# Performance work log

Measured on AMD Instinct MI355X. Metric: run time of the kernel, lower is better.

## Reference

```python
import jax, jax.numpy as jnp
import numpy as np

INFERENCE_TH = 0.3


def setup_inputs() -> dict:
    key = jax.random.key(0)
    k1, k2 = jax.random.split(key)
    N, C, H, W, K = 16, 30, 128, 128, 1000
    # Shift logits down so sigmoid scores are sparse above the threshold (realistic detector output).
    sCls = jax.random.normal(k1, (N, C, H, W), dtype=jnp.float32) - 2.0
    sReg = jax.random.normal(k2, (N, C * 16, H, W), dtype=jnp.float32) * 0.1
    # Anchors on a stride-8 grid, 64x64 boxes, laid out row-major to match the [N,H,W,A,C] flatten order.
    ys, xs = jnp.meshgrid(jnp.arange(H, dtype=jnp.float32) * 8.0 + 4.0,
                          jnp.arange(W, dtype=jnp.float32) * 8.0 + 4.0, indexing='ij')
    cx = xs.reshape(-1); cy = ys.reshape(-1); s = 32.0
    anchors = jnp.stack([cx - s, cy - s, cx + s, cy + s], axis=-1)  # [HW, 4]
    return {"sCls": sCls, "sReg": sReg, "anchors": anchors, "top_k": K}


def reference(sCls, sReg, anchors, top_k):
    N, C, H, W = sCls.shape
    HW = H * W
    # permute_and_flatten: [N, A*C, H, W] -> [N, H*W*A, C]  (A == 1)
    cls = jax.nn.sigmoid(jnp.transpose(sCls, (0, 2, 3, 1)).reshape(N, HW, C))        # [N, HW, C]
    reg = jnp.transpose(sReg, (0, 2, 3, 1)).reshape(N, HW, C, 16)                    # [N, HW, C, 16]
    # candidate_inds nonzero ordering is (loc, class) row-major over [HW, C];
    # flat index = loc*C + class, so topk over the flat axis reproduces it.
    flat = cls.reshape(N, HW * C)
    masked = jnp.where(flat > INFERENCE_TH, flat, -1.0)
    topv, topi = jax.lax.top_k(masked, top_k)        # [N, K]
    valid = topv > INFERENCE_TH                      # emulates per_pre_ransac_top_n truncation
    loc = topi // C                                  # spatial location (per_loc)
    cls_id = topi % C                                # class id (per_class)
    per_reg = jnp.take_along_axis(reg.reshape(N, HW * C, 16), topi[..., None], axis=1)  # [N, K, 16]
    anc = anchors[loc]                               # [N, K, 4]
    wa = anc[..., 2] - anc[..., 0]
    ha = anc[..., 3] - anc[..., 1]
    ctr_x = 0.5 * (anc[..., 0] + anc[..., 2])
    ctr_y = 0.5 * (anc[..., 1] + anc[..., 3])
    # box_coder.decode: 8 keypoint x-offsets then 8 y-offsets, scaled by anchor size around its center
    det_x = per_reg[..., :8] * wa[..., None] + ctr_x[..., None]
    det_y = per_reg[..., 8:] * ha[..., None] + ctr_y[..., None]
    detections = jnp.concatenate([det_x, det_y], axis=-1)       # [N, K, 16]
    detections = jnp.where(valid[..., None], detections, 0.0)
    scores = jnp.where(valid, jnp.sqrt(jnp.maximum(topv, 0.0)), 0.0)   # torch.sqrt(per_cls)
    labels = jnp.where(valid, cls_id + 1, 0)                            # per_class + 1
    return detections, labels, scores
```

## Files before the change

kernel.cpp:

```cpp
#include <hip/hip_runtime.h>
#include <stdint.h>
#include <math.h>

#define THREADS 256
#define NBINS   2048
#define CAP     2048
#define SORTN   2048
#define C_CLS   30
#define H_      128
#define W_      128
#define HW_     (H_*W_)
#define PER_IMG (C_CLS*HW_)
#define TH      0.3f
#define XLO     -0.8473f
#define BIN_LO  -0.85f
#define BIN_HI  3.35f
#define BIN_SCALE ((float)NBINS / (BIN_HI - BIN_LO))

__device__ __forceinline__ float sigmoid_rn(float x) {
    return (float)(1.0 / (1.0 + exp(-(double)x)));
}

__device__ __forceinline__ int bin_of_x(float x) {
    int b = (int)((x - BIN_LO) * BIN_SCALE);
    if (b < 0) b = 0;
    if (b > NBINS - 1) b = NBINS - 1;
    return b;
}

__device__ __forceinline__ unsigned mapf(float x) {
    unsigned u = __float_as_uint(x);
    return (u & 0x80000000u) ? ~u : (u ^ 0x80000000u);
}
__device__ __forceinline__ float unmapf(unsigned m) {
    unsigned u = (m & 0x80000000u) ? (m ^ 0x80000000u) : ~m;
    return __uint_as_float(u);
}

__global__ void k_hist(const float4* __restrict__ sCls, int* __restrict__ hist, int tot4) {
    int i = blockIdx.x * blockDim.x + threadIdx.x;
    if (i >= tot4) return;
    float4 v = sCls[i];
    int n = (int)(((long long)i * 4) / PER_IMG);
    int* h = hist + n * NBINS;
    if (v.x > XLO) atomicAdd(&h[bin_of_x(v.x)], 1);
    if (v.y > XLO) atomicAdd(&h[bin_of_x(v.y)], 1);
    if (v.z > XLO) atomicAdd(&h[bin_of_x(v.z)], 1);
    if (v.w > XLO) atomicAdd(&h[bin_of_x(v.w)], 1);
}

__global__ void k_cutoff(const int* __restrict__ hist, int* __restrict__ cutoffs, int K) {
    __shared__ int suf[NBINS];
    __shared__ int tot[THREADS];
    int n = blockIdx.x, t = threadIdx.x;
    const int CH = NBINS / THREADS;
    int base = t * CH;
    int run = 0;
    for (int i = CH - 1; i >= 0; --i) {
        run += hist[n * NBINS + base + i];
        suf[base + i] = run;
    }
    int myTot = run;
    tot[t] = run;
    __syncthreads();
    for (int d = 1; d < THREADS; d <<= 1) {
        int v = (t + d < THREADS) ? tot[t + d] : 0;
        __syncthreads();
        tot[t] += v;
        __syncthreads();
    }
    int add = tot[t] - myTot;
    for (int i = 0; i < CH; ++i) suf[base + i] += add;
    __syncthreads();
    if (t == 0 && suf[0] < K) cutoffs[n] = 0;
    for (int i = 0; i < CH; ++i) {
        int b = base + i;
        int sb = suf[b];
        int sb1 = (b + 1 < NBINS) ? suf[b + 1] : 0;
        if (sb >= K && sb1 < K) cutoffs[n] = b;
    }
}

__global__ void k_collect(const float4* __restrict__ sCls,
                          const int* __restrict__ cutoffs,
                          int* __restrict__ cnt,
                          unsigned long long* __restrict__ coll, int tot4) {
    __shared__ int lcnt;
    __shared__ int lbase;
    int i   = blockIdx.x * blockDim.x + threadIdx.x;
    int tid = threadIdx.x;
    int nblk = (int)(((long long)blockIdx.x * blockDim.x * 4) / PER_IMG);
    if (tid == 0) lcnt = 0;
    __syncthreads();

    int nq = 0;
    unsigned long long keys[4];
    int slot0 = 0;
    if (i < tot4) {
        float4 v = sCls[i];
        int r4 = i * 4;
        int co = cutoffs[nblk];
        int ri = r4 - nblk * PER_IMG;
        float xs[4] = {v.x, v.y, v.z, v.w};
        #pragma unroll
        for (int j = 0; j < 4; ++j) {
            float x = xs[j];
            if (x > XLO && bin_of_x(x) >= co) {
                int rr = ri + j;
                int c  = rr >> 14;
                int hw = rr & (HW_ - 1);
                int idx = hw * C_CLS + c;
                keys[nq] = ((unsigned long long)mapf(x) << 32) | (unsigned)(~idx);
                ++nq;
            }
        }
        if (nq) slot0 = atomicAdd(&lcnt, nq);
    }
    __syncthreads();
    if (tid == 0) lbase = (lcnt > 0) ? atomicAdd(&cnt[nblk], lcnt) : 0;
    __syncthreads();
    for (int j = 0; j < nq; ++j) {
        int s = lbase + slot0 + j;
        if (s < CAP) coll[nblk * CAP + s] = keys[j];
    }
}

__global__ __launch_bounds__(1024) void k_sort_decode(
        const unsigned long long* __restrict__ coll,
        const int* __restrict__ cnt,
        const float* __restrict__ sReg,
        const float* __restrict__ anchors,
        float* __restrict__ out, int N, int K) {
    __shared__ unsigned long long a[SORTN];
    int n = blockIdx.x, t = threadIdx.x;
    int m = cnt[n]; if (m > CAP) m = CAP;
    for (int i = t; i < SORTN; i += blockDim.x)
        a[i] = (i < m) ? coll[n * CAP + i] : 0ULL;
    __syncthreads();
    for (int k = 2; k <= SORTN; k <<= 1) {
        for (int j = k >> 1; j > 0; j >>= 1) {
            for (int i = t; i < SORTN; i += blockDim.x) {
                int l = i ^ j;
                if (l > i) {
                    unsigned long long ai = a[i], al = a[l];
                    bool up = ((i & k) == 0);
                    bool sw = up ? (ai < al) : (ai > al);
                    if (sw) { a[i] = al; a[l] = ai; }
                }
            }
            __syncthreads();
        }
    }
    float* det    = out;
    float* labels = out + (size_t)N * K * 16;
    float* scores = labels + (size_t)N * K;
    for (int kk = t; kk < K; kk += blockDim.x) {
        unsigned long long key = a[kk];
        float x = unmapf((unsigned)(key >> 32));
        float s = sigmoid_rn(x);
        float* drow = det + (size_t)(n * K + kk) * 16;
        if (s > TH) {
            int idx = (int)(~(unsigned int)key);
            int loc = idx / C_CLS;
            int c   = idx - loc * C_CLS;
            float a0 = anchors[loc * 4 + 0], a1 = anchors[loc * 4 + 1];
            float a2 = anchors[loc * 4 + 2], a3 = anchors[loc * 4 + 3];
            float wa = a2 - a0, ha = a3 - a1;
            float cx = 0.5f * (a0 + a2), cy = 0.5f * (a1 + a3);
            const float* rbase = sReg + (size_t)((n * C_CLS + c) * 16) * HW_ + loc;
            #pragma unroll
            for (int j = 0; j < 8; ++j)
                drow[j] = rbase[(size_t)j * HW_] * wa + cx;
            #pragma unroll
            for (int j = 0; j < 8; ++j)
                drow[8 + j] = rbase[(size_t)(8 + j) * HW_] * ha + cy;
            labels[n * K + kk] = (float)(c + 1);
            scores[n * K + kk] = sqrtf(s);
        } else {
            #pragma unroll
            for (int j = 0; j < 16; ++j) drow[j] = 0.0f;
            labels[n * K + kk] = 0.0f;
            scores[n * K + kk] = 0.0f;
        }
    }
}

extern "C" void kernel_launch(void* const* d_in, const int* in_sizes, int n_in,
                              void* d_out, int out_size, void* d_ws, size_t ws_size,
                              hipStream_t stream) {
    const float* sCls    = (const float*)d_in[0];
    const float* sReg    = (const float*)d_in[1];
    const float* anchors = (const float*)d_in[2];
    int tot = in_sizes[0];
    int N   = tot / PER_IMG;
    int K   = out_size / (N * 18);

    size_t hist_bytes = (size_t)N * NBINS * sizeof(int);
    char* ws = (char*)d_ws;
    int* hist    = (int*)ws;
    int* cnt     = (int*)(ws + hist_bytes);
    int* cutoffs = cnt + N;
    size_t coll_off = ((hist_bytes + (size_t)N * 8) + 255) & ~(size_t)255;
    unsigned long long* coll = (unsigned long long*)(ws + coll_off);

    hipMemsetAsync(d_ws, 0, coll_off, stream);

    int tot4 = tot / 4;
    int blocks4 = (tot4 + THREADS - 1) / THREADS;
    k_hist<<<blocks4, THREADS, 0, stream>>>((const float4*)sCls, hist, tot4);
    k_cutoff<<<N, THREADS, 0, stream>>>(hist, cutoffs, K);
    k_collect<<<blocks4, THREADS, 0, stream>>>((const float4*)sCls, cutoffs, cnt, coll, tot4);
    k_sort_decode<<<N, 1024, 0, stream>>>(coll, cnt, sReg, anchors, (float*)d_out, N, K);
}
```

Baseline: 895.1 us.

## Fuse histogram and candidate collection into one pass; split sort and decode

The histogram pass now also writes every above-threshold score key into a large per-image pre-candidate buffer. This removes the second full read of the class logits that the separate collect kernel needed. The sort kernel applies the cutoff bin while filtering those pre-candidates into shared memory before the bitonic sort, and decoding moves to its own grid-wide kernel instead of 16 blocks. In exchange it writes a much larger candidate buffer (about 8 bytes per above-threshold element), and its fixed per-image capacity sits close to the expected candidate count.

Measured after the change: 825.3 us. 7.8% less time.

```diff
diff --git a/kernel.cpp b/kernel.cpp
--- a/kernel.cpp
+++ b/kernel.cpp
@@ -4,8 +4,8 @@
 
 #define THREADS 256
 #define NBINS   2048
-#define CAP     2048
 #define SORTN   2048
+#define PRECAP  65536
 #define C_CLS   30
 #define H_      128
 #define W_      128
@@ -37,16 +37,48 @@
     return __uint_as_float(u);
 }
 
-__global__ void k_hist(const float4* __restrict__ sCls, int* __restrict__ hist, int tot4) {
-    int i = blockIdx.x * blockDim.x + threadIdx.x;
-    if (i >= tot4) return;
-    float4 v = sCls[i];
-    int n = (int)(((long long)i * 4) / PER_IMG);
-    int* h = hist + n * NBINS;
-    if (v.x > XLO) atomicAdd(&h[bin_of_x(v.x)], 1);
-    if (v.y > XLO) atomicAdd(&h[bin_of_x(v.y)], 1);
-    if (v.z > XLO) atomicAdd(&h[bin_of_x(v.z)], 1);
-    if (v.w > XLO) atomicAdd(&h[bin_of_x(v.w)], 1);
+__global__ void k_hist_collect(const float4* __restrict__ sCls,
+                               int* __restrict__ hist,
+                               int* __restrict__ cnt,
+                               unsigned long long* __restrict__ cand, int tot4) {
+    __shared__ int lcnt;
+    __shared__ int lbase;
+    int i   = blockIdx.x * blockDim.x + threadIdx.x;
+    int tid = threadIdx.x;
+    int n = (int)(((long long)blockIdx.x * blockDim.x * 4) / PER_IMG);
+    if (tid == 0) lcnt = 0;
+    __syncthreads();
+
+    int nq = 0;
+    unsigned long long keys[4];
+    int slot0 = 0;
+    if (i < tot4) {
+        float4 v = sCls[i];
+        int ri = i * 4 - n * PER_IMG;
+        int* h = hist + n * NBINS;
+        float xs[4] = {v.x, v.y, v.z, v.w};
+        #pragma unroll
+        for (int j = 0; j < 4; ++j) {
+            float x = xs[j];
+            if (x > XLO) {
+                atomicAdd(&h[bin_of_x(x)], 1);
+                int rr = ri + j;
+                int c  = rr >> 14;
+                int hw = rr & (HW_ - 1);
+                int idx = hw * C_CLS + c;
+                keys[nq] = ((unsigned long long)mapf(x) << 32) | (unsigned)(~idx);
+                ++nq;
+            }
+        }
+        if (nq) slot0 = atomicAdd(&lcnt, nq);
+    }
+    __syncthreads();
+    if (tid == 0) lbase = (lcnt > 0) ? atomicAdd(&cnt[n], lcnt) : 0;
+    __syncthreads();
+    for (int j = 0; j < nq; ++j) {
+        int s = lbase + slot0 + j;
+        if (s < PRECAP) cand[(size_t)n * PRECAP + s] = keys[j];
+    }
 }
 
 __global__ void k_cutoff(const int* __restrict__ hist, int* __restrict__ cutoffs, int K) {
@@ -81,61 +113,27 @@
     }
 }
 
-__global__ void k_collect(const float4* __restrict__ sCls,
-                          const int* __restrict__ cutoffs,
-                          int* __restrict__ cnt,
-                          unsigned long long* __restrict__ coll, int tot4) {
+__global__ __launch_bounds__(1024) void k_sort(
+        const unsigned long long* __restrict__ cand,
+        const int* __restrict__ cnt,
+        const int* __restrict__ cutoffs,
+        unsigned long long* __restrict__ topk, int K) {
+    __shared__ unsigned long long a[SORTN];
     __shared__ int lcnt;
-    __shared__ int lbase;
-    int i   = blockIdx.x * blockDim.x + threadIdx.x;
-    int tid = threadIdx.x;
-    int nblk = (int)(((long long)blockIdx.x * blockDim.x * 4) / PER_IMG);
-    if (tid == 0) lcnt = 0;
-    __syncthreads();
-
-    int nq = 0;
-    unsigned long long keys[4];
-    int slot0 = 0;
-    if (i < tot4) {
-        float4 v = sCls[i];
-        int r4 = i * 4;
-        int co = cutoffs[nblk];
-        int ri = r4 - nblk * PER_IMG;
-        float xs[4] = {v.x, v.y, v.z, v.w};
-        #pragma unroll
-        for (int j = 0; j < 4; ++j) {
-            float x = xs[j];
-            if (x > XLO && bin_of_x(x) >= co) {
-                int rr = ri + j;
-                int c  = rr >> 14;
-                int hw = rr & (HW_ - 1);
-                int idx = hw * C_CLS + c;
-                keys[nq] = ((unsigned long long)mapf(x) << 32) | (unsigned)(~idx);
-                ++nq;
-            }
+    int n = blockIdx.x, t = threadIdx.x;
+    if (t == 0) lcnt = 0;
+    for (int i = t; i < SORTN; i += blockDim.x) a[i] = 0ULL;
+    __syncthreads();
+    int m = cnt[n]; if (m > PRECAP) m = PRECAP;
+    int co = cutoffs[n];
+    for (int i = t; i < m; i += blockDim.x) {
+        unsigned long long key = cand[(size_t)n * PRECAP + i];
+        float x = unmapf((unsigned)(key >> 32));
+        if (bin_of_x(x) >= co) {
+            int s = atomicAdd(&lcnt, 1);
+            if (s < SORTN) a[s] = key;
         }
-        if (nq) slot0 = atomicAdd(&lcnt, nq);
-    }
-    __syncthreads();
-    if (tid == 0) lbase = (lcnt > 0) ? atomicAdd(&cnt[nblk], lcnt) : 0;
-    __syncthreads();
-    for (int j = 0; j < nq; ++j) {
-        int s = lbase + slot0 + j;
-        if (s < CAP) coll[nblk * CAP + s] = keys[j];
-    }
-}
-
-__global__ __launch_bounds__(1024) void k_sort_decode(
-        const unsigned long long* __restrict__ coll,
-        const int* __restrict__ cnt,
-        const float* __restrict__ sReg,
-        const float* __restrict__ anchors,
-        float* __restrict__ out, int N, int K) {
-    __shared__ unsigned long long a[SORTN];
-    int n = blockIdx.x, t = threadIdx.x;
-    int m = cnt[n]; if (m > CAP) m = CAP;
-    for (int i = t; i < SORTN; i += blockDim.x)
-        a[i] = (i < m) ? coll[n * CAP + i] : 0ULL;
+    }
     __syncthreads();
     for (int k = 2; k <= SORTN; k <<= 1) {
         for (int j = k >> 1; j > 0; j >>= 1) {
@@ -151,37 +149,46 @@
             __syncthreads();
         }
     }
+    for (int i = t; i < K; i += blockDim.x) topk[n * SORTN + i] = a[i];
+}
+
+__global__ void k_decode(const unsigned long long* __restrict__ topk,
+                         const float* __restrict__ sReg,
+                         const float* __restrict__ anchors,
+                         float* __restrict__ out, int N, int K) {
+    int i = blockIdx.x * blockDim.x + threadIdx.x;
+    if (i >= N * K) return;
+    int n = i / K;
+    int kk = i - n * K;
+    unsigned long long key = topk[n * SORTN + kk];
+    float x = unmapf((unsigned)(key >> 32));
+    float s = sigmoid_rn(x);
     float* det    = out;
     float* labels = out + (size_t)N * K * 16;
     float* scores = labels + (size_t)N * K;
-    for (int kk = t; kk < K; kk += blockDim.x) {
-        unsigned long long key = a[kk];
-        float x = unmapf((unsigned)(key >> 32));
-        float s = sigmoid_rn(x);
-        float* drow = det + (size_t)(n * K + kk) * 16;
-        if (s > TH) {
-            int idx = (int)(~(unsigned int)key);
-            int loc = idx / C_CLS;
-            int c   = idx - loc * C_CLS;
-            float a0 = anchors[loc * 4 + 0], a1 = anchors[loc * 4 + 1];
-            float a2 = anchors[loc * 4 + 2], a3 = anchors[loc * 4 + 3];
-            float wa = a2 - a0, ha = a3 - a1;
-            float cx = 0.5f * (a0 + a2), cy = 0.5f * (a1 + a3);
-            const float* rbase = sReg + (size_t)((n * C_CLS + c) * 16) * HW_ + loc;
-            #pragma unroll
-            for (int j = 0; j < 8; ++j)
-                drow[j] = rbase[(size_t)j * HW_] * wa + cx;
-            #pragma unroll
-            for (int j = 0; j < 8; ++j)
-                drow[8 + j] = rbase[(size_t)(8 + j) * HW_] * ha + cy;
-            labels[n * K + kk] = (float)(c + 1);
-            scores[n * K + kk] = sqrtf(s);
-        } else {
-            #pragma unroll
-            for (int j = 0; j < 16; ++j) drow[j] = 0.0f;
-            labels[n * K + kk] = 0.0f;
-            scores[n * K + kk] = 0.0f;
-        }
+    float* drow = det + (size_t)i * 16;
+    if (s > TH) {
+        int idx = (int)(~(unsigned int)key);
+        int loc = idx / C_CLS;
+        int c   = idx - loc * C_CLS;
+        float a0 = anchors[loc * 4 + 0], a1 = anchors[loc * 4 + 1];
+        float a2 = anchors[loc * 4 + 2], a3 = anchors[loc * 4 + 3];
+        float wa = a2 - a0, ha = a3 - a1;
+        float cx = 0.5f * (a0 + a2), cy = 0.5f * (a1 + a3);
+        const float* rbase = sReg + (size_t)((n * C_CLS + c) * 16) * HW_ + loc;
+        #pragma unroll
+        for (int j = 0; j < 8; ++j)
+            drow[j] = rbase[(size_t)j * HW_] * wa + cx;
+        #pragma unroll
+        for (int j = 0; j < 8; ++j)
+            drow[8 + j] = rbase[(size_t)(8 + j) * HW_] * ha + cy;
+        labels[i] = (float)(c + 1);
+        scores[i] = sqrtf(s);
+    } else {
+        #pragma unroll
+        for (int j = 0; j < 16; ++j) drow[j] = 0.0f;
+        labels[i] = 0.0f;
+        scores[i] = 0.0f;
     }
 }
 
@@ -195,20 +202,24 @@
     int N   = tot / PER_IMG;
     int K   = out_size / (N * 18);
 
+    char* ws = (char*)d_ws;
     size_t hist_bytes = (size_t)N * NBINS * sizeof(int);
-    char* ws = (char*)d_ws;
     int* hist    = (int*)ws;
     int* cnt     = (int*)(ws + hist_bytes);
     int* cutoffs = cnt + N;
-    size_t coll_off = ((hist_bytes + (size_t)N * 8) + 255) & ~(size_t)255;
-    unsigned long long* coll = (unsigned long long*)(ws + coll_off);
-
-    hipMemsetAsync(d_ws, 0, coll_off, stream);
+    size_t zero_bytes = hist_bytes + 2 * (size_t)N * sizeof(int);
+    size_t cand_off = (zero_bytes + 255) & ~(size_t)255;
+    unsigned long long* cand = (unsigned long long*)(ws + cand_off);
+    size_t topk_off = cand_off + (size_t)N * PRECAP * sizeof(unsigned long long);
+    unsigned long long* topk = (unsigned long long*)(ws + topk_off);
+
+    hipMemsetAsync(d_ws, 0, zero_bytes, stream);
 
     int tot4 = tot / 4;
     int blocks4 = (tot4 + THREADS - 1) / THREADS;
-    k_hist<<<blocks4, THREADS, 0, stream>>>((const float4*)sCls, hist, tot4);
+    k_hist_collect<<<blocks4, THREADS, 0, stream>>>((const float4*)sCls, hist, cnt, cand, tot4);
     k_cutoff<<<N, THREADS, 0, stream>>>(hist, cutoffs, K);
-    k_collect<<<blocks4, THREADS, 0, stream>>>((const float4*)sCls, cutoffs, cnt, coll, tot4);
-    k_sort_decode<<<N, 1024, 0, stream>>>(coll, cnt, sReg, anchors, (float*)d_out, N, K);
-}
+    k_sort<<<N, 1024, 0, stream>>>(cand, cnt, cutoffs, topk, K);
+    int nk = N * K;
+    k_decode<<<(nk + 255) / 256, 256, 0, stream>>>(topk, sReg, anchors, (float*)d_out, N, K);
+}
```
